# Optimization experiments

Hardware: AMD Instinct MI355X
Metric: run time of the kernel (lower is better)

The kernel has to match this reference:

```python
import jax, jax.numpy as jnp
import numpy as np

B, N, D = 8, 2048, 512
DK, DV = 512, 512


def setup_inputs() -> dict:
    key = jax.random.key(0)
    ks = jax.random.split(key, 7)
    s = 1.0 / np.sqrt(D)
    return {
        "x": jax.random.normal(ks[0], (B, N, D), dtype=jnp.float32),
        "Wq": jax.random.normal(ks[1], (D, DK), dtype=jnp.float32) * s,
        "bq": jnp.zeros((DK,), dtype=jnp.float32),
        "Wk": jax.random.normal(ks[2], (D, DK), dtype=jnp.float32) * s,
        "bk": jnp.zeros((DK,), dtype=jnp.float32),
        "Wv": jax.random.normal(ks[3], (D, DV), dtype=jnp.float32) * s,
        "bv": jnp.zeros((DV,), dtype=jnp.float32),
    }


def reference(x, Wq, bq, Wk, bk, Wv, bv):
    # norm = 1/sqrt(dim_k); original divides softmax output by norm (post-softmax scale)
    inv_norm = jnp.sqrt(jnp.asarray(DK, dtype=x.dtype))  # 1/norm = sqrt(dim_k)
    Q = x @ Wq + bq  # [B,N,DK]
    K = x @ Wk + bk  # [B,N,DK]
    V = x @ Wv + bv  # [B,N,DV]
    scores = jnp.einsum("bnd,bmd->bnm", Q, K)  # [B,N,N] (NO pre-softmax scaling)
    att = jax.nn.softmax(scores, axis=-1) * inv_norm  # faithful post-softmax scale
    return jnp.einsum("bnm,bmv->bnv", att, V)  # [B,N,DV]
```

## Files before the change

### kernel.cpp

```cpp
#include <hip/hip_runtime.h>
#include <stdint.h>
#include <stddef.h>


typedef _Float16 f16_t;
typedef _Float16 f16x8 __attribute__((ext_vector_type(8)));
typedef float    f32x4 __attribute__((ext_vector_type(4)));

__device__ __forceinline__ f32x4 mfma_h(f16x8 a, f16x8 b, f32x4 c) {
  return __builtin_amdgcn_mfma_f32_16x16x32_f16(a, b, c, 0, 0, 0);
}

__device__ __forceinline__ void gl_lds16(const void* g, void* lds) {
  __builtin_amdgcn_global_load_lds(
      (const __attribute__((address_space(1))) unsigned int*)g,
      (__attribute__((address_space(3))) unsigned int*)lds, 16, 0, 0);
}

__device__ __forceinline__ void stage_tile(f16_t* lds, const f16_t* g,
                                           size_t gstride, int wave, int lane) {
  const int l8 = lane >> 3;
  const int lslot = (lane & 7) ^ l8;
  #pragma unroll
  for (int c = 0; c < 4; ++c) {
    const int chunk = wave * 4 + c;
    const int row = chunk * 8 + l8;
    gl_lds16(g + (size_t)row * gstride + lslot * 8, lds + chunk * 512);
  }
}

__device__ __forceinline__ void stage128_8w(f16_t* lds, const f16_t* g,
                                            size_t gstride, int wave, int lane) {
  const int l8 = lane >> 3;
  const int lslot = (lane & 7) ^ l8;
  #pragma unroll
  for (int c = 0; c < 2; ++c) {
    const int chunk = wave * 2 + c;
    const int row = chunk * 8 + l8;
    gl_lds16(g + (size_t)row * gstride + lslot * 8, lds + chunk * 512);
  }
}

__device__ __forceinline__ void stage256_8w(f16_t* lds, const f16_t* g,
                                            size_t gstride, int wave, int lane) {
  const int l8 = lane >> 3;
  const int lslot = (lane & 7) ^ l8;
  #pragma unroll
  for (int c = 0; c < 4; ++c) {
    const int chunk = wave * 4 + c;
    const int row = chunk * 8 + l8;
    gl_lds16(g + (size_t)row * gstride + lslot * 8, lds + chunk * 512);
  }
}

__device__ __forceinline__ f16x8 lds_frag(const f16_t* buf, int R, int slot) {
  return *(const f16x8*)&buf[R * 64 + (((slot ^ (R & 7)) & 7) << 3)];
}

__device__ __forceinline__ int xcd_swz(int id, int nwg) {
  return (id & 7) * (nwg >> 3) + (id >> 3);
}

__global__ __launch_bounds__(256) void k_conv_x(const float* __restrict__ x,
                                                f16_t* __restrict__ x16) {
  const int i = (blockIdx.x * 256 + threadIdx.x) * 8;
  const float4 a = *(const float4*)&x[i];
  const float4 b = *(const float4*)&x[i + 4];
  float v[8] = {a.x, a.y, a.z, a.w, b.x, b.y, b.z, b.w};
  f16x8 h;
  #pragma unroll
  for (int j = 0; j < 8; ++j) h[j] = (f16_t)v[j];
  *(f16x8*)&x16[i] = h;
}

__global__ __launch_bounds__(256) void k_conv_w(const float* __restrict__ Wq,
                                                const float* __restrict__ Wk,
                                                const float* __restrict__ Wv,
                                                f16_t* __restrict__ Wt) {
  __shared__ float t[64][65];
  const int p = blockIdx.z;
  const float* __restrict__ W = (p == 0) ? Wq : (p == 1) ? Wk : Wv;
  const int n0 = blockIdx.x * 64, k0 = blockIdx.y * 64;
  const int tx = threadIdx.x & 63, ty = threadIdx.x >> 6;
  #pragma unroll
  for (int j = 0; j < 16; ++j)
    t[ty * 16 + j][tx] = W[(size_t)(k0 + ty * 16 + j) * 512 + n0 + tx];
  __syncthreads();
  #pragma unroll
  for (int j = 0; j < 16; ++j) {
    const int nl = ty * 16 + j;
    Wt[(size_t)p * 262144 + (size_t)(n0 + nl) * 512 + k0 + tx] =
        (f16_t)t[tx][nl];
  }
}

__global__ __launch_bounds__(256, 2) void k_proj(
    const f16_t* __restrict__ x16, const f16_t* __restrict__ Wt,
    const float* __restrict__ bq, const float* __restrict__ bk,
    const float* __restrict__ bv,
    f16_t* __restrict__ Q, f16_t* __restrict__ K, f16_t* __restrict__ Vt)
{
  __shared__ __align__(16) unsigned char smem[34816];
  f16_t* A = (f16_t*)smem;
  f16_t* B = (f16_t*)(smem + 16384);

  const int wg = xcd_swz(blockIdx.x, 1536);
  const int mt = wg / 12, jt = wg % 12;
  const int which = jt >> 2;
  const int jb = (jt & 3) * 128;

  const int tid = threadIdx.x, lane = tid & 63, wave = tid >> 6;
  const int wr = wave >> 1, wc = wave & 1, l15 = lane & 15, lg = lane >> 4;
  const int rowbase = mt * 128;

  const f16_t* Wbase = Wt + (size_t)which * 262144 + (size_t)jb * 512;

  f32x4 acc[4][4] = {};

  for (int kb = 0; kb < 512; kb += 64) {
    __syncthreads();
    stage_tile(A, x16 + (size_t)rowbase * 512 + kb, 512, wave, lane);
    stage_tile(B, Wbase + kb, 512, wave, lane);
    __syncthreads();
    #pragma unroll
    for (int h = 0; h < 2; ++h) {
      const int slot0 = h * 4 + lg;
      f16x8 af[4], bf[4];
      #pragma unroll
      for (int g = 0; g < 4; ++g) {
        af[g] = lds_frag(A, wr * 64 + g * 16 + l15, slot0);
        bf[g] = lds_frag(B, wc * 64 + g * 16 + l15, slot0);
      }
      #pragma unroll
      for (int i = 0; i < 4; ++i)
        #pragma unroll
        for (int j = 0; j < 4; ++j)
          acc[i][j] = mfma_h(af[i], bf[j], acc[i][j]);
    }
  }

  if (which != 2) {
    f16_t* __restrict__ O = (which == 0) ? Q : K;
    const float* __restrict__ bb = (which == 0) ? bq : bk;
    #pragma unroll
    for (int j = 0; j < 4; ++j) {
      const int jl = jb + wc * 64 + j * 16 + l15;
      const float bias = bb[jl];
      #pragma unroll
      for (int i = 0; i < 4; ++i)
        #pragma unroll
        for (int r = 0; r < 4; ++r) {
          const int row = rowbase + wr * 64 + i * 16 + lg * 4 + r;
          O[(size_t)row * 512 + jl] = (f16_t)(acc[i][j][r] + bias);
        }
    }
  } else {
    __syncthreads();
    f16_t* vtl = (f16_t*)smem;
    #pragma unroll
    for (int j = 0; j < 4; ++j) {
      const int jj = wc * 64 + j * 16 + l15;
      const float bias = bv[jb + jj];
      #pragma unroll
      for (int i = 0; i < 4; ++i)
        #pragma unroll
        for (int r = 0; r < 4; ++r) {
          const int ii = wr * 64 + i * 16 + lg * 4 + r;
          vtl[jj * 136 + ii] = (f16_t)(acc[i][j][r] + bias);
        }
    }
    __syncthreads();
    const int dv = tid >> 1, hf = tid & 1;
    const int bat = rowbase >> 11, n0 = rowbase & 2047;
    f16_t* __restrict__ dst =
        &Vt[((size_t)bat * 512 + jb + dv) * 2048 + n0 + hf * 64];
    const f16_t* src = &vtl[dv * 136 + hf * 64];
    #pragma unroll
    for (int s = 0; s < 8; ++s)
      *(f16x8*)&dst[s * 8] = *(const f16x8*)&src[s * 8];
  }
}

__global__ __launch_bounds__(256, 2) void k_qk2(const f16_t* __restrict__ Q,
                                                const f16_t* __restrict__ K,
                                                f16_t* __restrict__ P,
                                                float* __restrict__ mG,
                                                float* __restrict__ lG)
{
  __shared__ __align__(16) unsigned char smem[34816];
  f16_t* A  = (f16_t*)smem;
  f16_t* Bt = (f16_t*)(smem + 16384);

  const int wg = xcd_swz(blockIdx.x, 2048);
  const int bat = wg >> 8, mt = (wg >> 4) & 15, nt = wg & 15;
  const int tid = threadIdx.x, lane = tid & 63, wave = tid >> 6;
  const int wr = wave >> 1, wc = wave & 1, l15 = lane & 15, lg = lane >> 4;

  f32x4 acc[4][4] = {};
  const f16_t* Abase = Q + ((size_t)bat * 2048 + mt * 128) * 512;
  const f16_t* Bbase = K + ((size_t)bat * 2048 + nt * 128) * 512;

  for (int kb = 0; kb < 512; kb += 64) {
    __syncthreads();
    stage_tile(A, Abase + kb, 512, wave, lane);
    stage_tile(Bt, Bbase + kb, 512, wave, lane);
    __syncthreads();
    #pragma unroll
    for (int h = 0; h < 2; ++h) {
      const int slot0 = h * 4 + lg;
      f16x8 af[4], bf[4];
      #pragma unroll
      for (int g = 0; g < 4; ++g) {
        af[g] = lds_frag(A, wr * 64 + g * 16 + l15, slot0);
        bf[g] = lds_frag(Bt, wc * 64 + g * 16 + l15, slot0);
      }
      #pragma unroll
      for (int i = 0; i < 4; ++i)
        #pragma unroll
        for (int j = 0; j < 4; ++j)
          acc[i][j] = mfma_h(af[i], bf[j], acc[i][j]);
    }
  }

  __syncthreads();
  f16_t* Pl = (f16_t*)smem;
  const float LOG2E = 1.4426950408889634f;
  #pragma unroll
  for (int i = 0; i < 4; ++i)
    #pragma unroll
    for (int r = 0; r < 4; ++r) {
      const int rl = wr * 64 + i * 16 + lg * 4 + r;
      float mv = fmaxf(fmaxf(acc[i][0][r], acc[i][1][r]),
                       fmaxf(acc[i][2][r], acc[i][3][r]));
      mv = fmaxf(mv, __shfl_xor(mv, 1));
      mv = fmaxf(mv, __shfl_xor(mv, 2));
      mv = fmaxf(mv, __shfl_xor(mv, 4));
      mv = fmaxf(mv, __shfl_xor(mv, 8));
      float sum = 0.f;
      #pragma unroll
      for (int j = 0; j < 4; ++j) {
        const float e = __builtin_amdgcn_exp2f((acc[i][j][r] - mv) * LOG2E);
        Pl[rl * 136 + wc * 64 + j * 16 + l15] = (f16_t)e;
        sum += e;
      }
      sum += __shfl_xor(sum, 1);
      sum += __shfl_xor(sum, 2);
      sum += __shfl_xor(sum, 4);
      sum += __shfl_xor(sum, 8);
      if (l15 == 0) {
        const size_t idx =
            ((size_t)(bat * 32 + nt * 2 + wc)) * 2048 + mt * 128 + rl;
        mG[idx] = mv;
        lG[idx] = sum;
      }
    }
  __syncthreads();

  {
    const int row = tid >> 1, half = tid & 1;
    f16_t* __restrict__ dst =
        P + ((size_t)bat * 2048 + mt * 128 + row) * 2048 + nt * 128 + half * 64;
    const f16_t* src = &Pl[row * 136 + half * 64];
    #pragma unroll
    for (int s = 0; s < 8; ++s)
      *(f16x8*)&dst[s * 8] = *(const f16x8*)&src[s * 8];
  }
}

__global__ __launch_bounds__(512, 1) void k_pv6(const f16_t* __restrict__ P,
                                                const f16_t* __restrict__ Vt,
                                                const float* __restrict__ mG,
                                                const float* __restrict__ lG,
                                                float* __restrict__ out)
{
  __shared__ __align__(16) f16_t Pl[128 * 64];
  __shared__ __align__(16) f16_t Vl[256 * 64];
  __shared__ f16_t facL[128][34];
  __shared__ float scrow[128];
  __shared__ float redp[128][4];

  const int id = blockIdx.x;
  const int bat = id & 7, qt = (id >> 3) & 15, dvh = id >> 7;
  const int tid = threadIdx.x, lane = tid & 63, wave = tid >> 6;
  const int l15 = lane & 15, lg = lane >> 4;
  const int wq = wave >> 2, wd = wave & 3;
  const float LOG2E = 1.4426950408889634f;

  {
    const int prow = tid >> 2, part = tid & 3;
    float mt8[8], lt8[8];
    #pragma unroll
    for (int s = 0; s < 8; ++s) {
      const size_t idx =
          ((size_t)(bat * 32 + part * 8 + s)) * 2048 + qt * 128 + prow;
      mt8[s] = mG[idx];
      lt8[s] = lG[idx];
    }
    float mm = mt8[0];
    #pragma unroll
    for (int s = 1; s < 8; ++s) mm = fmaxf(mm, mt8[s]);
    redp[prow][part] = mm;
    __syncthreads();
    const float M = fmaxf(fmaxf(redp[prow][0], redp[prow][1]),
                          fmaxf(redp[prow][2], redp[prow][3]));
    __syncthreads();
    float ls = 0.f;
    #pragma unroll
    for (int s = 0; s < 8; ++s) {
      const float f = __builtin_amdgcn_exp2f((mt8[s] - M) * LOG2E);
      facL[prow][part * 8 + s] = (f16_t)f;
      ls += lt8[s] * f;
    }
    redp[prow][part] = ls;
    __syncthreads();
    if (part == 0)
      scrow[prow] = 22.62741699796952f /
                    (redp[prow][0] + redp[prow][1] + redp[prow][2] + redp[prow][3]);
  }

  const f16_t* Pbase = P + ((size_t)bat * 2048 + qt * 128) * 2048;
  const f16_t* Vbase = Vt + ((size_t)bat * 512 + dvh * 256) * 2048;

  f32x4 acc[4][4] = {};

  for (int t = 0; t < 32; ++t) {
    __syncthreads();
    stage128_8w(Pl, Pbase + t * 64, 2048, wave, lane);
    stage256_8w(Vl, Vbase + t * 64, 2048, wave, lane);
    __syncthreads();
    f16_t fv[4];
    #pragma unroll
    for (int g = 0; g < 4; ++g) fv[g] = facL[wq * 64 + g * 16 + l15][t];
    #pragma unroll
    for (int ks = 0; ks < 2; ++ks) {
      const int slot0 = ks * 4 + lg;
      f16x8 af[4], bf[4];
      #pragma unroll
      for (int g = 0; g < 4; ++g) {
        af[g] = lds_frag(Pl, wq * 64 + g * 16 + l15, slot0) * fv[g];
        bf[g] = lds_frag(Vl, wd * 64 + g * 16 + l15, slot0);
      }
      #pragma unroll
      for (int i = 0; i < 4; ++i)
        #pragma unroll
        for (int j = 0; j < 4; ++j)
          acc[i][j] = mfma_h(af[i], bf[j], acc[i][j]);
    }
  }

  #pragma unroll
  for (int i = 0; i < 4; ++i)
    #pragma unroll
    for (int r = 0; r < 4; ++r) {
      const int ql = wq * 64 + i * 16 + lg * 4 + r;
      const float sc = scrow[ql];
      const size_t orow = ((size_t)bat * 2048 + qt * 128 + ql) * 512;
      #pragma unroll
      for (int j = 0; j < 4; ++j) {
        const int dv = dvh * 256 + wd * 64 + j * 16 + l15;
        out[orow + dv] = acc[i][j][r] * sc;
      }
    }
}

extern "C" void kernel_launch(void* const* d_in, const int* in_sizes, int n_in,
                              void* d_out, int out_size, void* d_ws, size_t ws_size,
                              hipStream_t stream) {
  const float* x  = (const float*)d_in[0];
  const float* Wq = (const float*)d_in[1];
  const float* bq = (const float*)d_in[2];
  const float* Wk = (const float*)d_in[3];
  const float* bk = (const float*)d_in[4];
  const float* Wv = (const float*)d_in[5];
  const float* bv = (const float*)d_in[6];
  float* out = (float*)d_out;

  char* ws = (char*)d_ws;
  f16_t* x16 = (f16_t*)(ws + 0);
  f16_t* Q   = (f16_t*)(ws + 16777216);
  f16_t* K   = (f16_t*)(ws + 33554432);
  f16_t* Vt  = (f16_t*)(ws + 50331648);
  f16_t* P   = (f16_t*)(ws + 67108864);
  float* mG  = (float*)(ws + 134217728);
  float* lG  = (float*)(ws + 136314880);
  f16_t* Wt  = (f16_t*)(ws + 201326592);

  k_conv_x<<<4096, 256, 0, stream>>>(x, x16);
  k_conv_w<<<dim3(8, 8, 3), 256, 0, stream>>>(Wq, Wk, Wv, Wt);
  k_proj<<<1536, 256, 0, stream>>>(x16, Wt, bq, bk, bv, Q, K, Vt);
  k_qk2<<<2048, 256, 0, stream>>>(Q, K, P, mG, lG);
  k_pv6<<<256, 512, 0, stream>>>(P, Vt, mG, lG, out);
}
```

Baseline: 167.1 us.

## Store P as contiguous 128x128 tiles and split PV kernel into smaller blocks

The QK kernel now writes each 128x128 probability tile contiguously instead of into a row-major NxN matrix. The PV kernel reads those tiles with a 128-element stride. The PV kernel also moves from 256 blocks of 512 threads over 128 query rows to 512 blocks of 256 threads over 64 query rows, with two blocks per CU allowed. The aim is better DRAM locality for P loads and more blocks for occupancy across CUs, at the cost of each V tile being loaded twice as often.

```diff
diff --git a/kernel.cpp b/kernel.cpp
--- a/kernel.cpp
+++ b/kernel.cpp
@@ -29,25 +29,13 @@
   }
 }
 
-__device__ __forceinline__ void stage128_8w(f16_t* lds, const f16_t* g,
-                                            size_t gstride, int wave, int lane) {
+__device__ __forceinline__ void stage_tile64(f16_t* lds, const f16_t* g,
+                                             size_t gstride, int wave, int lane) {
   const int l8 = lane >> 3;
   const int lslot = (lane & 7) ^ l8;
   #pragma unroll
   for (int c = 0; c < 2; ++c) {
     const int chunk = wave * 2 + c;
-    const int row = chunk * 8 + l8;
-    gl_lds16(g + (size_t)row * gstride + lslot * 8, lds + chunk * 512);
-  }
-}
-
-__device__ __forceinline__ void stage256_8w(f16_t* lds, const f16_t* g,
-                                            size_t gstride, int wave, int lane) {
-  const int l8 = lane >> 3;
-  const int lslot = (lane & 7) ^ l8;
-  #pragma unroll
-  for (int c = 0; c < 4; ++c) {
-    const int chunk = wave * 4 + c;
     const int row = chunk * 8 + l8;
     gl_lds16(g + (size_t)row * gstride + lslot * 8, lds + chunk * 512);
   }
@@ -257,33 +245,34 @@
   __syncthreads();
 
   {
-    const int row = tid >> 1, half = tid & 1;
     f16_t* __restrict__ dst =
-        P + ((size_t)bat * 2048 + mt * 128 + row) * 2048 + nt * 128 + half * 64;
-    const f16_t* src = &Pl[row * 136 + half * 64];
-    #pragma unroll
-    for (int s = 0; s < 8; ++s)
-      *(f16x8*)&dst[s * 8] = *(const f16x8*)&src[s * 8];
-  }
-}
-
-__global__ __launch_bounds__(512, 1) void k_pv6(const f16_t* __restrict__ P,
+        P + (((size_t)(bat * 16 + mt) * 16 + nt) << 14);
+    const int c16 = tid & 15, r0 = tid >> 4;
+    #pragma unroll
+    for (int s = 0; s < 8; ++s) {
+      const int row = s * 16 + r0;
+      *(f16x8*)&dst[row * 128 + c16 * 8] =
+          *(const f16x8*)&Pl[row * 136 + c16 * 8];
+    }
+  }
+}
+
+__global__ __launch_bounds__(256, 2) void k_pv7(const f16_t* __restrict__ P,
                                                 const f16_t* __restrict__ Vt,
                                                 const float* __restrict__ mG,
                                                 const float* __restrict__ lG,
                                                 float* __restrict__ out)
 {
-  __shared__ __align__(16) f16_t Pl[128 * 64];
+  __shared__ __align__(16) f16_t Pl[64 * 64];
   __shared__ __align__(16) f16_t Vl[256 * 64];
-  __shared__ f16_t facL[128][34];
-  __shared__ float scrow[128];
-  __shared__ float redp[128][4];
+  __shared__ f16_t facL[64][34];
+  __shared__ float scrow[64];
+  __shared__ float redp[64][4];
 
   const int id = blockIdx.x;
-  const int bat = id & 7, qt = (id >> 3) & 15, dvh = id >> 7;
+  const int bat = id & 7, qt = (id >> 3) & 31, dvh = id >> 8;
   const int tid = threadIdx.x, lane = tid & 63, wave = tid >> 6;
   const int l15 = lane & 15, lg = lane >> 4;
-  const int wq = wave >> 2, wd = wave & 3;
   const float LOG2E = 1.4426950408889634f;
 
   {
@@ -292,7 +281,7 @@
     #pragma unroll
     for (int s = 0; s < 8; ++s) {
       const size_t idx =
-          ((size_t)(bat * 32 + part * 8 + s)) * 2048 + qt * 128 + prow;
+          ((size_t)(bat * 32 + part * 8 + s)) * 2048 + qt * 64 + prow;
       mt8[s] = mG[idx];
       lt8[s] = lG[idx];
     }
@@ -318,27 +307,33 @@
                     (redp[prow][0] + redp[prow][1] + redp[prow][2] + redp[prow][3]);
   }
 
-  const f16_t* Pbase = P + ((size_t)bat * 2048 + qt * 128) * 2048;
+  const int mtq = qt >> 1;
+  const int rowhalf = (qt & 1) * 64;
+  const f16_t* Ptiles = P + (((size_t)(bat * 16 + mtq)) << 18);
   const f16_t* Vbase = Vt + ((size_t)bat * 512 + dvh * 256) * 2048;
 
   f32x4 acc[4][4] = {};
 
   for (int t = 0; t < 32; ++t) {
     __syncthreads();
-    stage128_8w(Pl, Pbase + t * 64, 2048, wave, lane);
-    stage256_8w(Vl, Vbase + t * 64, 2048, wave, lane);
+    const f16_t* psrc =
+        Ptiles + ((size_t)(t >> 1) << 14) + rowhalf * 128 + (t & 1) * 64;
+    stage_tile64(Pl, psrc, 128, wave, lane);
+    stage_tile(Vl, Vbase + t * 64, 2048, wave, lane);
+    stage_tile(Vl + 128 * 64, Vbase + (size_t)128 * 2048 + t * 64, 2048,
+               wave, lane);
     __syncthreads();
     f16_t fv[4];
     #pragma unroll
-    for (int g = 0; g < 4; ++g) fv[g] = facL[wq * 64 + g * 16 + l15][t];
+    for (int g = 0; g < 4; ++g) fv[g] = facL[g * 16 + l15][t];
     #pragma unroll
     for (int ks = 0; ks < 2; ++ks) {
       const int slot0 = ks * 4 + lg;
       f16x8 af[4], bf[4];
       #pragma unroll
       for (int g = 0; g < 4; ++g) {
-        af[g] = lds_frag(Pl, wq * 64 + g * 16 + l15, slot0) * fv[g];
-        bf[g] = lds_frag(Vl, wd * 64 + g * 16 + l15, slot0);
+        af[g] = lds_frag(Pl, g * 16 + l15, slot0) * fv[g];
+        bf[g] = lds_frag(Vl, wave * 64 + g * 16 + l15, slot0);
       }
       #pragma unroll
       for (int i = 0; i < 4; ++i)
@@ -352,12 +347,12 @@
   for (int i = 0; i < 4; ++i)
     #pragma unroll
     for (int r = 0; r < 4; ++r) {
-      const int ql = wq * 64 + i * 16 + lg * 4 + r;
+      const int ql = i * 16 + lg * 4 + r;
       const float sc = scrow[ql];
-      const size_t orow = ((size_t)bat * 2048 + qt * 128 + ql) * 512;
+      const size_t orow = ((size_t)bat * 2048 + qt * 64 + ql) * 512;
       #pragma unroll
       for (int j = 0; j < 4; ++j) {
-        const int dv = dvh * 256 + wd * 64 + j * 16 + l15;
+        const int dv = dvh * 256 + wave * 64 + j * 16 + l15;
         out[orow + dv] = acc[i][j][r] * sc;
       }
     }
@@ -389,5 +384,5 @@
   k_conv_w<<<dim3(8, 8, 3), 256, 0, stream>>>(Wq, Wk, Wv, Wt);
   k_proj<<<1536, 256, 0, stream>>>(x16, Wt, bq, bk, bv, Q, K, Vt);
   k_qk2<<<2048, 256, 0, stream>>>(Q, K, P, mG, lG);
-  k_pv6<<<256, 512, 0, stream>>>(P, Vt, mG, lG, out);
-}
+  k_pv7<<<512, 256, 0, stream>>>(P, Vt, mG, lG, out);
+}
```

Result: faster. 147.3 us (-11.8%).
